# Kernel optimization log

Measured on AMD Instinct MI355X. Metric: run time of the kernel, lower is better.

## Reference

```python
import jax, jax.numpy as jnp
import numpy as np

N_NODES = 200_000
N_EDGES = 400_000
EXTRA_NNZ = 3 * N_EDGES
IN_CH = 14
HID = 128
ALPHA = -1.5  # HNHN edge-cardinality exponent
BETA = -0.5   # HNHN node-cardinality exponent


def setup_inputs() -> dict:
    key = jax.random.key(0)
    ks = jax.random.split(key, 16)
    # COO incidence: guarantee every node and every edge has >= 1 entry so
    # cardinality^negative_power stays finite (like real molecular hypergraphs).
    base_rows = jnp.arange(N_NODES, dtype=jnp.int32)
    base_cols = jnp.arange(N_NODES, dtype=jnp.int32) % N_EDGES
    edge_rows = jax.random.randint(ks[0], (N_EDGES,), 0, N_NODES, dtype=jnp.int32)
    edge_cols = jnp.arange(N_EDGES, dtype=jnp.int32)
    rnd_rows = jax.random.randint(ks[1], (EXTRA_NNZ,), 0, N_NODES, dtype=jnp.int32)
    rnd_cols = jax.random.randint(ks[2], (EXTRA_NNZ,), 0, N_EDGES, dtype=jnp.int32)
    inc_rows = jnp.concatenate([base_rows, edge_rows, rnd_rows])
    inc_cols = jnp.concatenate([base_cols, edge_cols, rnd_cols])
    inc_vals = jnp.ones(inc_rows.shape[0], dtype=jnp.float32)

    def glorot(k, shape):
        fan_in, fan_out = shape[0], shape[-1]
        s = jnp.sqrt(2.0 / (fan_in + fan_out)).astype(jnp.float32)
        return jax.random.normal(k, shape, dtype=jnp.float32) * s

    return {
        "x_0": jax.random.normal(ks[3], (N_NODES, IN_CH), dtype=jnp.float32),
        "inc_rows": inc_rows,
        "inc_cols": inc_cols,
        "inc_vals": inc_vals,
        "w0_l1": glorot(ks[4], (IN_CH, HID)),
        "w1_l1": glorot(ks[5], (HID, HID)),
        "b1_l1": glorot(ks[6], (1, HID)),
        "b0_l1": glorot(ks[7], (1, HID)),
        "w0_l2": glorot(ks[8], (HID, HID)),
        "w1_l2": glorot(ks[9], (HID, HID)),
        "b1_l2": glorot(ks[10], (1, HID)),
        "b0_l2": glorot(ks[11], (1, HID)),
        "lin_w": glorot(ks[12], (HID, 1)),
        "lin_b": jnp.zeros((1,), dtype=jnp.float32),
    }


def _normalized_values(inc_rows, inc_cols, inc_vals):
    """HNHN alpha/beta normalization of B (node<-edge) and B^T (edge<-node)."""
    seg = jax.ops.segment_sum
    deg_e = seg(inc_vals, inc_cols, num_segments=N_EDGES)   # |e| per hyperedge
    deg_v = seg(inc_vals, inc_rows, num_segments=N_NODES)   # |v| per node
    e_card = deg_e ** ALPHA
    n_card = deg_v ** BETA
    denom_v = seg(inc_vals * e_card[inc_cols], inc_rows, num_segments=N_NODES)  # (B @ e_card)
    denom_e = seg(inc_vals * n_card[inc_rows], inc_cols, num_segments=N_EDGES)  # (B^T @ n_card)
    # D0_left_alpha^{-1} B D1_right_alpha   and   D1_left_beta^{-1} B^T D0_right_beta
    vals_v_from_e = inc_vals * e_card[inc_cols] / denom_v[inc_rows]
    vals_e_from_v = inc_vals * n_card[inc_rows] / denom_e[inc_cols]
    return vals_v_from_e, vals_e_from_v


def reference(x_0, inc_rows, inc_cols, inc_vals,
              w0_l1, w1_l1, b1_l1, b0_l1,
              w0_l2, w1_l2, b1_l2, b0_l2,
              lin_w, lin_b):
    seg = jax.ops.segment_sum
    vals_v_from_e, vals_e_from_v = _normalized_values(inc_rows, inc_cols, inc_vals)

    def layer(x0, w0, w1, b1, b0):
        # node -> hyperedge: x1 = sigma(Bt_norm @ (x0 W0) + b1)
        m = x0 @ w0                                        # [N_NODES, HID]
        x1 = jax.nn.sigmoid(
            seg(vals_e_from_v[:, None] * m[inc_rows], inc_cols, num_segments=N_EDGES) + b1
        )                                                  # [N_EDGES, HID]
        # hyperedge -> node: x0' = sigma(B_norm @ (x1 W1) + b0)
        m2 = x1 @ w1
        x0n = jax.nn.sigmoid(
            seg(vals_v_from_e[:, None] * m2[inc_cols], inc_rows, num_segments=N_NODES) + b0
        )                                                  # [N_NODES, HID]
        return x0n, x1

    x0, x1 = layer(x_0, w0_l1, w1_l1, b1_l1, b0_l1)
    x0, x1 = layer(x0, w0_l2, w1_l2, b1_l2, b0_l2)
    pooled = jnp.max(x0, axis=0)                           # graph-level max pool [HID]
    return pooled @ lin_w + lin_b                          # [1]
```

## Files before the change

### kernel.cpp

```cpp
#include <hip/hip_runtime.h>
#include <hip/hip_bf16.h>

#define N_NODES 200000
#define N_EDGES 400000
#define HID 128

#define SHIFT 10
#define NB_E 391
#define NB_V 196
#define NBT (NB_E + NB_V)

typedef unsigned int u32;
typedef unsigned short u16;
typedef unsigned char u8;
typedef long long i64;
typedef __attribute__((ext_vector_type(4))) float f32x4;
typedef __attribute__((ext_vector_type(2))) float f32x2;

__device__ inline float sigmoidf(float v) { return 1.0f / (1.0f + __expf(-v)); }

__device__ inline u32 pk4_fp8(float f0, float f1, float f2, float f3) {
  u32 v = __builtin_amdgcn_cvt_pk_fp8_f32(f0, f1, 0, false);
  v = __builtin_amdgcn_cvt_pk_fp8_f32(f2, f3, v, true);
  return v;
}

__device__ inline void acc16_fp8(const uint4& q, float wv, float* a) {
#pragma unroll
  for (int h = 0; h < 4; ++h) {
    u32 u = (&q.x)[h];
    f32x2 p0 = __builtin_amdgcn_cvt_pk_f32_fp8(u, false);
    f32x2 p1 = __builtin_amdgcn_cvt_pk_f32_fp8(u, true);
    a[h * 4 + 0] = fmaf(wv, p0.x, a[h * 4 + 0]);
    a[h * 4 + 1] = fmaf(wv, p0.y, a[h * 4 + 1]);
    a[h * 4 + 2] = fmaf(wv, p1.x, a[h * 4 + 2]);
    a[h * 4 + 3] = fmaf(wv, p1.y, a[h * 4 + 3]);
  }
}


__global__ __launch_bounds__(256) void histA_kernel(
    const int* __restrict__ rows, const int* __restrict__ cols,
    u32* __restrict__ gcnt_e, u32* __restrict__ gcnt_v, int nnz) {
  __shared__ u32 h[NBT];
  const int tid = threadIdx.x;
  for (int j = tid; j < NBT; j += 256) h[j] = 0;
  __syncthreads();
  const int i0 = blockIdx.x * 2048;
#pragma unroll
  for (int k = 0; k < 8; ++k) {
    int i = i0 + k * 256 + tid;
    if (i < nnz) {
      atomicAdd(&h[cols[i] >> SHIFT], 1u);
      atomicAdd(&h[NB_E + (rows[i] >> SHIFT)], 1u);
    }
  }
  __syncthreads();
  for (int j = tid; j < NBT; j += 256) {
    u32 n = h[j];
    if (n) {
      if (j < NB_E) atomicAdd(&gcnt_e[j], n);
      else          atomicAdd(&gcnt_v[j - NB_E], n);
    }
  }
}

__global__ __launch_bounds__(512) void scan_small_kernel(u32* __restrict__ blk, int n) {
  __shared__ u32 tmp[512];
  int t = threadIdx.x;
  u32 v = (t < n) ? blk[t] : 0;
  tmp[t] = v;
  __syncthreads();
  for (int d = 1; d < 512; d <<= 1) {
    u32 x = (t >= d) ? tmp[t - d] : 0;
    __syncthreads();
    tmp[t] += x;
    __syncthreads();
  }
  if (t < n) blk[t] = tmp[t] - v;
}

__global__ void set4_kernel(u32* __restrict__ bbE, u32* __restrict__ bbV,
                            u32* __restrict__ ptr_e, u32* __restrict__ ptr_v,
                            u32 nnz) {
  bbE[NB_E] = nnz;
  bbV[NB_V] = nnz;
  ptr_e[N_EDGES] = nnz;
  ptr_v[N_NODES] = nnz;
}

__global__ __launch_bounds__(256) void bin_kernel(
    const int* __restrict__ rows, const int* __restrict__ cols,
    const float* __restrict__ vals, const u32* __restrict__ bbE,
    const u32* __restrict__ bbV, u32* __restrict__ gcur,
    int4* __restrict__ tmp_e, int4* __restrict__ tmp_v, int nnz) {
  __shared__ u32 h[NBT];
  __shared__ u32 base[NBT];
  __shared__ u32 bb[NBT];
  const int tid = threadIdx.x;
  for (int j = tid; j < NBT; j += 256) {
    h[j] = 0;
    bb[j] = (j < NB_E) ? bbE[j] : bbV[j - NB_E];
  }
  __syncthreads();
  const int i0 = blockIdx.x * 2048;
#pragma unroll
  for (int k = 0; k < 8; ++k) {
    int i = i0 + k * 256 + tid;
    if (i < nnz) {
      atomicAdd(&h[cols[i] >> SHIFT], 1u);
      atomicAdd(&h[NB_E + (rows[i] >> SHIFT)], 1u);
    }
  }
  __syncthreads();
  for (int j = tid; j < NBT; j += 256) {
    u32 n = h[j];
    base[j] = n ? atomicAdd(&gcur[j], n) : 0;
    h[j] = 0;
  }
  __syncthreads();
#pragma unroll
  for (int k = 0; k < 8; ++k) {
    int i = i0 + k * 256 + tid;
    if (i < nnz) {
      int c = cols[i], r = rows[i];
      int vb = __float_as_int(vals[i]);
      int be = c >> SHIFT;
      int bv = NB_E + (r >> SHIFT);
      u32 le = atomicAdd(&h[be], 1u);
      tmp_e[bb[be] + base[be] + le] = make_int4(c, r, vb, 0);
      u32 lv = atomicAdd(&h[bv], 1u);
      tmp_v[bb[bv] + base[bv] + lv] = make_int4(r, c, vb, 0);
    }
  }
}

template <bool EDGE>
__global__ __launch_bounds__(512) void build_kernel(
    const int4* __restrict__ tmp, const u32* __restrict__ bukBase,
    u32* __restrict__ ptr, int2* __restrict__ ent, float* __restrict__ card,
    int S) {
  __shared__ u32 loc[1024];
  __shared__ u32 sstart[1024];
  __shared__ u32 aux[512];
  const int tid = threadIdx.x;
  const int c0 = blockIdx.x << SHIFT;
  const int nseg = min(1024, S - c0);
  const u32 eb = bukBase[blockIdx.x], ee = bukBase[blockIdx.x + 1];
  loc[tid] = 0;
  loc[tid + 512] = 0;
  __syncthreads();
  for (u32 j = eb + tid; j < ee; j += 512)
    atomicAdd(&loc[tmp[j].x - c0], 1u);
  __syncthreads();
  u32 a0 = loc[2 * tid], a1 = loc[2 * tid + 1];
  u32 T = a0 + a1;
  aux[tid] = T;
  __syncthreads();
  for (int d = 1; d < 512; d <<= 1) {
    u32 x = (tid >= d) ? aux[tid - d] : 0;
    __syncthreads();
    aux[tid] += x;
    __syncthreads();
  }
  u32 off = aux[tid] - T;
  loc[2 * tid] = off;
  loc[2 * tid + 1] = off + a0;
  sstart[2 * tid] = off;
  sstart[2 * tid + 1] = off + a0;
  __syncthreads();
  for (int k = tid; k < nseg; k += 512) ptr[c0 + k] = eb + loc[k];
  __syncthreads();
  for (u32 j = eb + tid; j < ee; j += 512) {
    int4 e = tmp[j];
    u32 p = atomicAdd(&loc[e.x - c0], 1u);
    ent[eb + p] = make_int2(e.y, e.z);
  }
  __syncthreads();
  for (int k = tid; k < nseg; k += 512) {
    u32 s0 = sstart[k], s1 = loc[k];
    float s = 0.f;
    for (u32 j = s0; j < s1; ++j) s += __int_as_float(ent[eb + j].y);
    float t = rsqrtf(s);
    card[c0 + k] = EDGE ? t * t * t : t;
  }
}


__global__ __launch_bounds__(256) void segCD_kernel(
    const u32* __restrict__ ptr_e, int2* __restrict__ ent_e,
    const u32* __restrict__ ptr_v, int2* __restrict__ ent_v,
    const float* __restrict__ e_card, const float* __restrict__ n_card) {
  int i = blockIdx.x * 256 + threadIdx.x;
  if (i < N_EDGES) {
    u32 b = ptr_e[i], e = ptr_e[i + 1];
    float s = 0.f;
    for (u32 j = b; j < e; ++j) {
      int2 en = ent_e[j];
      s += __int_as_float(en.y) * n_card[en.x];
    }
    float inv = 1.f / s;
    for (u32 j = b; j < e; ++j) {
      int2 en = ent_e[j];
      ent_e[j].y = __float_as_int(__int_as_float(en.y) * n_card[en.x] * inv);
    }
  }
  if (i < N_NODES) {
    u32 b = ptr_v[i], e = ptr_v[i + 1];
    float s = 0.f;
    for (u32 j = b; j < e; ++j) {
      int2 en = ent_v[j];
      s += __int_as_float(en.y) * e_card[en.x];
    }
    float inv = 1.f / s;
    for (u32 j = b; j < e; ++j) {
      int2 en = ent_v[j];
      ent_v[j].y = __float_as_int(__int_as_float(en.y) * e_card[en.x] * inv);
    }
  }
}


__global__ __launch_bounds__(256) void mm14n_kernel(
    const float* __restrict__ x0, const float* __restrict__ w,
    u8* __restrict__ U, int N) {
  __shared__ float ws[14 * HID];
  const int tid = threadIdx.x;
  for (int i = tid; i < 14 * HID; i += 256) ws[i] = w[i];
  __syncthreads();
  const int row = blockIdx.x * 8 + (tid >> 5);
  const int c4 = (tid & 31) << 2;
  if (row >= N) return;
  const float* xr = x0 + (size_t)row * 14;
  float a0 = 0.f, a1 = 0.f, a2 = 0.f, a3 = 0.f;
#pragma unroll
  for (int k = 0; k < 14; ++k) {
    const float xv = xr[k];
    const float* wr = ws + k * HID + c4;
    a0 = fmaf(xv, wr[0], a0);
    a1 = fmaf(xv, wr[1], a1);
    a2 = fmaf(xv, wr[2], a2);
    a3 = fmaf(xv, wr[3], a3);
  }
  *(u32*)(U + (size_t)row * HID + c4) = pk4_fp8(a0, a1, a2, a3);
}

template <bool SIG, bool POOL>
__global__ __launch_bounds__(256, 1) void im128_mfma_kernel(
    u8* __restrict__ buf, const float* __restrict__ w,
    const float* __restrict__ b, u32* __restrict__ pooled, int R) {
  const int tid = threadIdx.x;
  const int wave = tid >> 6;
  const int lo = tid & 15;
  const int hi = (tid & 63) >> 4;
  i64 wf[8][4];
#pragma unroll
  for (int n = 0; n < 8; ++n)
#pragma unroll
    for (int t = 0; t < 4; ++t) {
      const float* wp = w + (size_t)(t * 32 + hi * 8) * HID + n * 16 + lo;
      u32 w0 = pk4_fp8(wp[0], wp[HID], wp[2 * HID], wp[3 * HID]);
      u32 w1 = pk4_fp8(wp[4 * HID], wp[5 * HID], wp[6 * HID], wp[7 * HID]);
      wf[n][t] = (i64)w0 | ((i64)w1 << 32);
    }
  float bias[8];
  if (SIG) {
#pragma unroll
    for (int n = 0; n < 8; ++n) bias[n] = b[n * 16 + lo];
  }
  float pm[8];
#pragma unroll
  for (int n = 0; n < 8; ++n) pm[n] = 0.f;

  for (int rb = blockIdx.x * 64 + wave * 16; rb < R; rb += gridDim.x * 64) {
    const u8* xp = buf + (size_t)(rb + lo) * HID + hi * 8;
    i64 a0 = *(const i64*)(xp);
    i64 a1 = *(const i64*)(xp + 32);
    i64 a2 = *(const i64*)(xp + 64);
    i64 a3 = *(const i64*)(xp + 96);
    u8* yp = buf + (size_t)(rb + hi * 4) * HID + lo;
#pragma unroll
    for (int n = 0; n < 8; ++n) {
      f32x4 c = {0.f, 0.f, 0.f, 0.f};
      c = __builtin_amdgcn_mfma_f32_16x16x32_fp8_fp8(a0, wf[n][0], c, 0, 0, 0);
      c = __builtin_amdgcn_mfma_f32_16x16x32_fp8_fp8(a1, wf[n][1], c, 0, 0, 0);
      c = __builtin_amdgcn_mfma_f32_16x16x32_fp8_fp8(a2, wf[n][2], c, 0, 0, 0);
      c = __builtin_amdgcn_mfma_f32_16x16x32_fp8_fp8(a3, wf[n][3], c, 0, 0, 0);
#pragma unroll
      for (int r = 0; r < 4; ++r) {
        float v = SIG ? sigmoidf(c[r] + bias[n]) : c[r];
        if (POOL) {
          pm[n] = fmaxf(pm[n], v);
        } else {
          u32 q = __builtin_amdgcn_cvt_pk_fp8_f32(v, v, 0, false);
          yp[(size_t)r * HID + n * 16] = (u8)q;
        }
      }
    }
  }

  if (POOL) {
    __shared__ u32 pmax[HID];
    for (int i = tid; i < HID; i += 256) pmax[i] = 0;
    __syncthreads();
#pragma unroll
    for (int n = 0; n < 8; ++n)
      atomicMax(&pmax[n * 16 + lo], __float_as_uint(pm[n]));
    __syncthreads();
    if (tid < HID) atomicMax(&pooled[tid], pmax[tid]);
  }
}


template <bool SIG>
__global__ __launch_bounds__(256) void gather128_kernel(
    const u32* __restrict__ ptr, const int2* __restrict__ ent,
    const u8* __restrict__ src, const float* __restrict__ b,
    u8* __restrict__ dst, int S) {
  long long t = (long long)blockIdx.x * 256 + threadIdx.x;
  int r = (int)(t >> 3);
  if (r >= S) return;
  const int c16 = (int)(t & 7) << 4;
  u32 beg = ptr[r], end = ptr[r + 1];
  float a[16];
#pragma unroll
  for (int i = 0; i < 16; ++i) a[i] = 0.f;
  u32 j = beg;
  for (; j + 2 <= end; j += 2) {
    int2 e0 = ent[j];
    int2 e1 = ent[j + 1];
    const uint4 q0 = *(const uint4*)(src + (size_t)e0.x * HID + c16);
    const uint4 q1 = *(const uint4*)(src + (size_t)e1.x * HID + c16);
    acc16_fp8(q0, __int_as_float(e0.y), a);
    acc16_fp8(q1, __int_as_float(e1.y), a);
  }
  if (j < end) {
    int2 e0 = ent[j];
    const uint4 q0 = *(const uint4*)(src + (size_t)e0.x * HID + c16);
    acc16_fp8(q0, __int_as_float(e0.y), a);
  }
  if (SIG) {
#pragma unroll
    for (int h = 0; h < 4; ++h) {
      float4 bb = *(const float4*)(b + c16 + h * 4);
      a[h * 4 + 0] = sigmoidf(a[h * 4 + 0] + bb.x);
      a[h * 4 + 1] = sigmoidf(a[h * 4 + 1] + bb.y);
      a[h * 4 + 2] = sigmoidf(a[h * 4 + 2] + bb.z);
      a[h * 4 + 3] = sigmoidf(a[h * 4 + 3] + bb.w);
    }
  }
  uint4 pk;
  pk.x = pk4_fp8(a[0], a[1], a[2], a[3]);
  pk.y = pk4_fp8(a[4], a[5], a[6], a[7]);
  pk.z = pk4_fp8(a[8], a[9], a[10], a[11]);
  pk.w = pk4_fp8(a[12], a[13], a[14], a[15]);
  *(uint4*)(dst + (size_t)r * HID + c16) = pk;
}


__global__ __launch_bounds__(128) void final_kernel(
    const u32* __restrict__ pooled, const float* __restrict__ lin_w,
    const float* __restrict__ lin_b, float* __restrict__ out) {
  __shared__ float red[64];
  int t = threadIdx.x;
  float v = __uint_as_float(pooled[t]) * lin_w[t];
  if (t >= 64) red[t - 64] = v;
  __syncthreads();
  if (t < 64) {
    v += red[t];
#pragma unroll
    for (int off = 32; off > 0; off >>= 1) v += __shfl_down(v, off);
    if (t == 0) out[0] = v + lin_b[0];
  }
}

__global__ void diag_kernel(float* out, float v) { out[0] = v; }


extern "C" void kernel_launch(void* const* d_in, const int* in_sizes, int n_in,
                              void* d_out, int out_size, void* d_ws, size_t ws_size,
                              hipStream_t stream) {
  const float* x0     = (const float*)d_in[0];
  const int*   rows   = (const int*)d_in[1];
  const int*   cols   = (const int*)d_in[2];
  const float* vals   = (const float*)d_in[3];
  const float* w0_l1  = (const float*)d_in[4];
  const float* w1_l1  = (const float*)d_in[5];
  const float* b1_l1  = (const float*)d_in[6];
  const float* b0_l1  = (const float*)d_in[7];
  const float* w0_l2  = (const float*)d_in[8];
  const float* w1_l2  = (const float*)d_in[9];
  const float* b1_l2  = (const float*)d_in[10];
  const float* b0_l2  = (const float*)d_in[11];
  const float* lin_w  = (const float*)d_in[12];
  const float* lin_b  = (const float*)d_in[13];
  float* out = (float*)d_out;
  const int nnz = in_sizes[1];

  char* wsp = (char*)d_ws;
  size_t off = 0;
  auto carve = [&](size_t bytes) -> char* {
    char* p = wsp + off;
    off = (off + bytes + 511) & ~(size_t)511;
    return p;
  };
  float* n_card  = (float*)carve((size_t)N_NODES * 4);
  float* e_card  = (float*)carve((size_t)N_EDGES * 4);
  u32*   ptr_v   = (u32*)carve((size_t)(N_NODES + 1) * 4);
  u32*   ptr_e   = (u32*)carve((size_t)(N_EDGES + 1) * 4);
  u32*   bbE     = (u32*)carve((NB_E + 1) * 4);
  u32*   bbV     = (u32*)carve((NB_V + 1) * 4);
  u32*   gcur    = (u32*)carve(NBT * 4);
  int2*  ent_v   = (int2*)carve((size_t)nnz * 8);
  int2*  ent_e   = (int2*)carve((size_t)nnz * 8);
  u32*   pooled  = (u32*)carve(HID * 4);
  u8*    bufN    = (u8*)carve((size_t)N_NODES * HID);
  u8*    bufE    = (u8*)carve((size_t)N_EDGES * HID);
  int4*  tmp_e   = (int4*)carve((size_t)nnz * 16);
  int4*  tmp_v   = (int4*)carve((size_t)nnz * 16);

  if (off > ws_size) {
    diag_kernel<<<1, 1, 0, stream>>>(out, (float)(ws_size >> 20));
    return;
  }

  hipMemsetAsync(bbE, 0, (NB_E + 1) * 4, stream);
  hipMemsetAsync(bbV, 0, (NB_V + 1) * 4, stream);
  hipMemsetAsync(gcur, 0, NBT * 4, stream);
  hipMemsetAsync(pooled, 0, HID * 4, stream);

  const int nbBin = (nnz + 2047) / 2048;

  histA_kernel<<<nbBin, 256, 0, stream>>>(rows, cols, bbE, bbV, nnz);
  scan_small_kernel<<<1, 512, 0, stream>>>(bbE, NB_E);
  scan_small_kernel<<<1, 512, 0, stream>>>(bbV, NB_V);
  set4_kernel<<<1, 1, 0, stream>>>(bbE, bbV, ptr_e, ptr_v, (u32)nnz);
  bin_kernel<<<nbBin, 256, 0, stream>>>(rows, cols, vals, bbE, bbV, gcur,
                                        tmp_e, tmp_v, nnz);
  build_kernel<true><<<NB_E, 512, 0, stream>>>(tmp_e, bbE, ptr_e, ent_e,
                                               e_card, N_EDGES);
  build_kernel<false><<<NB_V, 512, 0, stream>>>(tmp_v, bbV, ptr_v, ent_v,
                                                n_card, N_NODES);

  const int nbSeg = (N_EDGES + 255) / 256;
  segCD_kernel<<<nbSeg, 256, 0, stream>>>(ptr_e, ent_e, ptr_v, ent_v, e_card, n_card);

  const int nbE8 = (int)(((long long)N_EDGES * 8 + 255) / 256);
  const int nbN8 = (int)(((long long)N_NODES * 8 + 255) / 256);

  mm14n_kernel<<<N_NODES / 8, 256, 0, stream>>>(x0, w0_l1, bufN, N_NODES);
  gather128_kernel<true><<<nbE8, 256, 0, stream>>>(ptr_e, ent_e, bufN,
                                                   b1_l1, bufE, N_EDGES);
  gather128_kernel<false><<<nbN8, 256, 0, stream>>>(ptr_v, ent_v, bufE,
                                                    nullptr, bufN, N_NODES);
  im128_mfma_kernel<true, false><<<1024, 256, 0, stream>>>(bufN, w1_l1, b0_l1,
                                                           nullptr, N_NODES);

  im128_mfma_kernel<false, false><<<1024, 256, 0, stream>>>(bufN, w0_l2, nullptr,
                                                            nullptr, N_NODES);
  gather128_kernel<true><<<nbE8, 256, 0, stream>>>(ptr_e, ent_e, bufN,
                                                   b1_l2, bufE, N_EDGES);
  gather128_kernel<false><<<nbN8, 256, 0, stream>>>(ptr_v, ent_v, bufE,
                                                    nullptr, bufN, N_NODES);
  im128_mfma_kernel<true, true><<<1024, 256, 0, stream>>>(bufN, w1_l2, b0_l2,
                                                          pooled, N_NODES);

  final_kernel<<<1, 128, 0, stream>>>(pooled, lin_w, lin_b, out);
}
```

Baseline: 524.0 us.

## Pack binned COO entries into int2 and fuse edge normalization into build

```diff
diff --git a/kernel.cpp b/kernel.cpp
--- a/kernel.cpp
+++ b/kernel.cpp
@@ -93,7 +93,7 @@
     const int* __restrict__ rows, const int* __restrict__ cols,
     const float* __restrict__ vals, const u32* __restrict__ bbE,
     const u32* __restrict__ bbV, u32* __restrict__ gcur,
-    int4* __restrict__ tmp_e, int4* __restrict__ tmp_v, int nnz) {
+    int2* __restrict__ tmp_e, int2* __restrict__ tmp_v, int nnz) {
   __shared__ u32 h[NBT];
   __shared__ u32 base[NBT];
   __shared__ u32 bb[NBT];
@@ -128,18 +128,18 @@
       int be = c >> SHIFT;
       int bv = NB_E + (r >> SHIFT);
       u32 le = atomicAdd(&h[be], 1u);
-      tmp_e[bb[be] + base[be] + le] = make_int4(c, r, vb, 0);
+      tmp_e[bb[be] + base[be] + le] = make_int2(((c & 1023) << 19) | r, vb);
       u32 lv = atomicAdd(&h[bv], 1u);
-      tmp_v[bb[bv] + base[bv] + lv] = make_int4(r, c, vb, 0);
+      tmp_v[bb[bv] + base[bv] + lv] = make_int2(((r & 1023) << 19) | c, vb);
     }
   }
 }
 
 template <bool EDGE>
 __global__ __launch_bounds__(512) void build_kernel(
-    const int4* __restrict__ tmp, const u32* __restrict__ bukBase,
+    const int2* __restrict__ tmp, const u32* __restrict__ bukBase,
     u32* __restrict__ ptr, int2* __restrict__ ent, float* __restrict__ card,
-    int S) {
+    const float* __restrict__ ncard, int S) {
   __shared__ u32 loc[1024];
   __shared__ u32 sstart[1024];
   __shared__ u32 aux[512];
@@ -151,7 +151,7 @@
   loc[tid + 512] = 0;
   __syncthreads();
   for (u32 j = eb + tid; j < ee; j += 512)
-    atomicAdd(&loc[tmp[j].x - c0], 1u);
+    atomicAdd(&loc[(u32)tmp[j].x >> 19], 1u);
   __syncthreads();
   u32 a0 = loc[2 * tid], a1 = loc[2 * tid + 1];
   u32 T = a0 + a1;
@@ -172,51 +172,48 @@
   for (int k = tid; k < nseg; k += 512) ptr[c0 + k] = eb + loc[k];
   __syncthreads();
   for (u32 j = eb + tid; j < ee; j += 512) {
-    int4 e = tmp[j];
-    u32 p = atomicAdd(&loc[e.x - c0], 1u);
-    ent[eb + p] = make_int2(e.y, e.z);
+    int2 e = tmp[j];
+    u32 s = (u32)e.x >> 19;
+    u32 p = atomicAdd(&loc[s], 1u);
+    ent[eb + p] = make_int2(e.x & 0x7FFFF, e.y);
   }
   __syncthreads();
   for (int k = tid; k < nseg; k += 512) {
-    u32 s0 = sstart[k], s1 = loc[k];
+    u32 s0 = eb + sstart[k], s1 = eb + loc[k];
     float s = 0.f;
-    for (u32 j = s0; j < s1; ++j) s += __int_as_float(ent[eb + j].y);
+    for (u32 j = s0; j < s1; ++j) s += __int_as_float(ent[j].y);
     float t = rsqrtf(s);
     card[c0 + k] = EDGE ? t * t * t : t;
-  }
-}
-
-
-__global__ __launch_bounds__(256) void segCD_kernel(
-    const u32* __restrict__ ptr_e, int2* __restrict__ ent_e,
+    if (EDGE) {
+      float d = 0.f;
+      for (u32 j = s0; j < s1; ++j) {
+        int2 en = ent[j];
+        d += __int_as_float(en.y) * ncard[en.x];
+      }
+      float inv = 1.f / d;
+      for (u32 j = s0; j < s1; ++j) {
+        int2 en = ent[j];
+        ent[j].y = __float_as_int(__int_as_float(en.y) * ncard[en.x] * inv);
+      }
+    }
+  }
+}
+
+__global__ __launch_bounds__(256) void segV_kernel(
     const u32* __restrict__ ptr_v, int2* __restrict__ ent_v,
-    const float* __restrict__ e_card, const float* __restrict__ n_card) {
+    const float* __restrict__ e_card) {
   int i = blockIdx.x * 256 + threadIdx.x;
-  if (i < N_EDGES) {
-    u32 b = ptr_e[i], e = ptr_e[i + 1];
-    float s = 0.f;
-    for (u32 j = b; j < e; ++j) {
-      int2 en = ent_e[j];
-      s += __int_as_float(en.y) * n_card[en.x];
-    }
-    float inv = 1.f / s;
-    for (u32 j = b; j < e; ++j) {
-      int2 en = ent_e[j];
-      ent_e[j].y = __float_as_int(__int_as_float(en.y) * n_card[en.x] * inv);
-    }
-  }
-  if (i < N_NODES) {
-    u32 b = ptr_v[i], e = ptr_v[i + 1];
-    float s = 0.f;
-    for (u32 j = b; j < e; ++j) {
-      int2 en = ent_v[j];
-      s += __int_as_float(en.y) * e_card[en.x];
-    }
-    float inv = 1.f / s;
-    for (u32 j = b; j < e; ++j) {
-      int2 en = ent_v[j];
-      ent_v[j].y = __float_as_int(__int_as_float(en.y) * e_card[en.x] * inv);
-    }
+  if (i >= N_NODES) return;
+  u32 b = ptr_v[i], e = ptr_v[i + 1];
+  float s = 0.f;
+  for (u32 j = b; j < e; ++j) {
+    int2 en = ent_v[j];
+    s += __int_as_float(en.y) * e_card[en.x];
+  }
+  float inv = 1.f / s;
+  for (u32 j = b; j < e; ++j) {
+    int2 en = ent_v[j];
+    ent_v[j].y = __float_as_int(__int_as_float(en.y) * e_card[en.x] * inv);
   }
 }
 
@@ -416,8 +413,8 @@
   u32*   pooled  = (u32*)carve(HID * 4);
   u8*    bufN    = (u8*)carve((size_t)N_NODES * HID);
   u8*    bufE    = (u8*)carve((size_t)N_EDGES * HID);
-  int4*  tmp_e   = (int4*)carve((size_t)nnz * 16);
-  int4*  tmp_v   = (int4*)carve((size_t)nnz * 16);
+  int2*  tmp_e   = (int2*)carve((size_t)nnz * 8);
+  int2*  tmp_v   = (int2*)carve((size_t)nnz * 8);
 
   if (off > ws_size) {
     diag_kernel<<<1, 1, 0, stream>>>(out, (float)(ws_size >> 20));
@@ -437,13 +434,11 @@
   set4_kernel<<<1, 1, 0, stream>>>(bbE, bbV, ptr_e, ptr_v, (u32)nnz);
   bin_kernel<<<nbBin, 256, 0, stream>>>(rows, cols, vals, bbE, bbV, gcur,
                                         tmp_e, tmp_v, nnz);
+  build_kernel<false><<<NB_V, 512, 0, stream>>>(tmp_v, bbV, ptr_v, ent_v,
+                                                n_card, nullptr, N_NODES);
   build_kernel<true><<<NB_E, 512, 0, stream>>>(tmp_e, bbE, ptr_e, ent_e,
-                                               e_card, N_EDGES);
-  build_kernel<false><<<NB_V, 512, 0, stream>>>(tmp_v, bbV, ptr_v, ent_v,
-                                                n_card, N_NODES);
-
-  const int nbSeg = (N_EDGES + 255) / 256;
-  segCD_kernel<<<nbSeg, 256, 0, stream>>>(ptr_e, ent_e, ptr_v, ent_v, e_card, n_card);
+                                               e_card, n_card, N_EDGES);
+  segV_kernel<<<(N_NODES + 255) / 256, 256, 0, stream>>>(ptr_v, ent_v, e_card);
 
   const int nbE8 = (int)(((long long)N_EDGES * 8 + 255) / 256);
   const int nbN8 = (int)(((long long)N_NODES * 8 + 255) / 256);
```

Result: faster. 509.9 us (-2.7%).
